# Kernel optimization log

Hardware: AMD Instinct MI355X
Metric: run time of the kernel (lower is better)

The kernel has to match this reference:

```python
import jax
import jax.numpy as jnp
from jax import lax
import numpy as np

B, N, NPOINT, NSAMPLE, C = 8, 8192, 2048, 32, 64
RADIUS = 0.2
BIG = jnp.float32(1e10)


def setup_inputs() -> dict:
    key = jax.random.key(0)
    ks = jax.random.split(key, 8)
    xyz = jax.random.uniform(ks[0], (B, N, 3), dtype=jnp.float32)          # points in unit cube
    features = jax.random.normal(ks[1], (B, C, N), dtype=jnp.float32)
    w1 = jax.random.normal(ks[2], (64, C + 3), dtype=jnp.float32) * 0.1
    b1 = jnp.zeros((64,), jnp.float32)
    w2 = jax.random.normal(ks[3], (64, 64), dtype=jnp.float32) * 0.1
    b2 = jnp.zeros((64,), jnp.float32)
    w3 = jax.random.normal(ks[4], (128, 64), dtype=jnp.float32) * 0.1
    b3 = jnp.zeros((128,), jnp.float32)
    return {"xyz": xyz, "features": features, "w1": w1, "b1": b1,
            "w2": w2, "b2": b2, "w3": w3, "b3": b3}


def _fps(xyz, npoint):
    """Furthest point sampling. xyz: (B,N,3) -> idx (B,npoint) int32."""
    def one(pts):  # (N,3)
        n = pts.shape[0]
        def step(carry, _):
            dist, far = carry
            d = jnp.sum((pts - pts[far]) ** 2, axis=-1)    # (N,)
            dist = jnp.minimum(dist, d)
            nxt = jnp.argmax(dist).astype(jnp.int32)
            return (dist, nxt), far
        init = (jnp.full((n,), BIG, pts.dtype), jnp.int32(0))
        _, idx = lax.scan(step, init, None, length=npoint)
        return idx
    return jax.vmap(one)(xyz)


def _ball_query(xyz, new_xyz, radius, nsample):
    """xyz (B,N,3), new_xyz (B,S,3) -> idx (B,S,nsample) int32, pointnet2 semantics:
    first nsample in-radius points in index order; pad with first hit."""
    n = xyz.shape[1]
    d2 = (jnp.sum(new_xyz ** 2, -1)[:, :, None]
          + jnp.sum(xyz ** 2, -1)[:, None, :]
          - 2.0 * jnp.einsum("bsd,bnd->bsn", new_xyz, xyz))  # (B,S,N)
    mask = d2 < radius * radius
    keys = jnp.where(mask, jnp.arange(n, dtype=jnp.int32)[None, None, :], jnp.int32(n))
    idx = jnp.sort(keys, axis=-1)[..., :nsample]             # (B,S,nsample)
    first = idx[..., :1]
    idx = jnp.where(idx >= n, first, idx)
    idx = jnp.where(idx >= n, 0, idx)                        # degenerate: no neighbor at all
    return idx


def _conv_bn_relu(h, w, b):
    # 1x1 Conv2d over (B, Cin, S, ns) with folded BN -> ReLU
    return jax.nn.relu(jnp.einsum("oc,bcps->bops", w, h) + b[None, :, None, None])


def _forward(xyz, features, w1, b1, w2, b2, w3, b3):
    fps_idx = _fps(xyz, NPOINT)                                          # (B,S)
    new_xyz = jnp.take_along_axis(xyz, fps_idx[:, :, None], axis=1)      # (B,S,3)
    idx = _ball_query(xyz, new_xyz, RADIUS, NSAMPLE)                     # (B,S,ns)
    b, s, ns = idx.shape
    flat = idx.reshape(b, s * ns)
    grouped_xyz = jnp.take_along_axis(xyz, flat[:, :, None], axis=1).reshape(b, s, ns, 3)
    grouped_xyz = grouped_xyz - new_xyz[:, :, None, :]                   # center
    grouped_xyz = jnp.transpose(grouped_xyz, (0, 3, 1, 2))               # (B,3,S,ns)
    grouped_feat = jnp.take_along_axis(features, flat[:, None, :], axis=2).reshape(b, C, s, ns)
    h = jnp.concatenate([grouped_xyz, grouped_feat], axis=1)             # (B,3+C,S,ns)
    h = _conv_bn_relu(h, w1, b1)
    h = _conv_bn_relu(h, w2, b2)
    h = _conv_bn_relu(h, w3, b3)
    new_features = jnp.max(h, axis=-1)                                   # (B,128,S)
    return new_xyz, new_features


def reference(xyz, features, w1, b1, w2, b2, w3, b3):
    return _forward(xyz, features, w1, b1, w2, b2, w3, b3)
```

## Files before the change

### kernel.cpp

```cpp
#include <hip/hip_runtime.h>
#include <stdint.h>

#define NB 8
#define NN 8192
#define NP 2048
#define NSAMP 32
#define NC 64

typedef float v2f __attribute__((ext_vector_type(2)));

__global__ __launch_bounds__(256) void prep_kernel(
    const float* __restrict__ w1, const float* __restrict__ w2,
    const float* __restrict__ w3, float* __restrict__ w1t,
    float* __restrict__ w2t, float* __restrict__ w3t)
{
    int j = blockIdx.x * 256 + threadIdx.x;
    if (j < 64*67) { int o = j / 67, k = j % 67; w1t[k*64 + o] = w1[j]; }
    int j2 = j - 64*67;
    if (j2 >= 0 && j2 < 64*64) { int o = j2 >> 6, k = j2 & 63; w2t[k*64 + o] = w2[j2]; }
    int j3 = j2 - 64*64;
    if (j3 >= 0 && j3 < 128*64) { int o = j3 >> 6, k = j3 & 63; w3t[k*128 + o] = w3[j3]; }
}

#define DPP_MAXF(m, CTRL) do { \
    int _s = __builtin_amdgcn_update_dpp(__float_as_int(m), __float_as_int(m), \
                                         CTRL, 0xf, 0xf, false); \
    float _f = __int_as_float(_s); \
    m = fmaxf(m, _f); } while (0)

#define DPP_MINI(c, CTRL) do { \
    int _s = __builtin_amdgcn_update_dpp(c, c, CTRL, 0xf, 0xf, false); \
    c = (_s < c) ? _s : c; } while (0)

__global__ __launch_bounds__(512) void fps_kernel(
    const float* __restrict__ xyz, int* __restrict__ fps_idx,
    float* __restrict__ out_newxyz)
{
#pragma clang fp contract(off)
    __shared__ float sxyz[NN * 3];
    __shared__ float bv[2][8];
    __shared__ int   bix[2][8];

    const int b = blockIdx.x;
    const int t = threadIdx.x;
    const int lane = t & 63;
    const int w = t >> 6;
    const float* base = xyz + (size_t)b * NN * 3;

    for (int i = t; i < NN * 3 / 4; i += 512)
        ((float4*)sxyz)[i] = ((const float4*)base)[i];
    __syncthreads();

    const int p0 = t * 16;
    v2f X[8], Y[8], Z[8], D[8];
    #pragma unroll
    for (int j = 0; j < 8; j++) {
        int pa = p0 + 2*j, pb = p0 + 2*j + 1;
        X[j] = (v2f){ sxyz[pa*3+0], sxyz[pb*3+0] };
        Y[j] = (v2f){ sxyz[pa*3+1], sxyz[pb*3+1] };
        Z[j] = (v2f){ sxyz[pa*3+2], sxyz[pb*3+2] };
        D[j] = (v2f){ 1e10f, 1e10f };
    }

    int far = 0;
    for (int k = 0; k < NP; k++) {
        float fx = sxyz[far * 3 + 0];
        float fy = sxyz[far * 3 + 1];
        float fz = sxyz[far * 3 + 2];
        if (t == 0) {
            fps_idx[b * NP + k] = far;
            out_newxyz[((size_t)b * NP + k) * 3 + 0] = fx;
            out_newxyz[((size_t)b * NP + k) * 3 + 1] = fy;
            out_newxyz[((size_t)b * NP + k) * 3 + 2] = fz;
        }

        v2f fx2 = { fx, fx }, fy2 = { fy, fy }, fz2 = { fz, fz };
        #pragma unroll
        for (int j = 0; j < 8; j++) {
            v2f dx = X[j] - fx2;
            v2f dy = Y[j] - fy2;
            v2f dz = Z[j] - fz2;
            v2f d  = (dx*dx + dy*dy) + dz*dz;
            D[j].x = fminf(D[j].x, d.x);
            D[j].y = fminf(D[j].y, d.y);
        }

        float m0 = fmaxf(fmaxf(D[0].x, D[0].y), D[1].x);
        float m1 = fmaxf(fmaxf(D[1].y, D[2].x), D[2].y);
        float m2 = fmaxf(fmaxf(D[3].x, D[3].y), D[4].x);
        float m3 = fmaxf(fmaxf(D[4].y, D[5].x), D[5].y);
        float m4 = fmaxf(fmaxf(D[6].x, D[6].y), D[7].x);
        float m  = fmaxf(fmaxf(fmaxf(m0, m1), fmaxf(m2, m3)),
                         fmaxf(m4, D[7].y));

        DPP_MAXF(m, 0x111); DPP_MAXF(m, 0x112); DPP_MAXF(m, 0x114);
        DPP_MAXF(m, 0x118); DPP_MAXF(m, 0x142); DPP_MAXF(m, 0x143);
        float wm = __int_as_float(__builtin_amdgcn_readlane(__float_as_int(m), 63));

        int cand = 0x7FFFFFFF;
        #pragma unroll
        for (int j = 7; j >= 0; j--) {
            if (D[j].y == wm) cand = p0 + 2*j + 1;
            if (D[j].x == wm) cand = p0 + 2*j;
        }
        DPP_MINI(cand, 0x111); DPP_MINI(cand, 0x112); DPP_MINI(cand, 0x114);
        DPP_MINI(cand, 0x118); DPP_MINI(cand, 0x142); DPP_MINI(cand, 0x143);
        int widx = __builtin_amdgcn_readlane(cand, 63);

        if (lane == 0) { bv[k & 1][w] = wm; bix[k & 1][w] = widx; }
        __syncthreads();

        float gv = bv[k & 1][0]; int gi = bix[k & 1][0];
        #pragma unroll
        for (int ww = 1; ww < 8; ww++) {
            float v = bv[k & 1][ww]; int i = bix[k & 1][ww];
            if (v > gv) { gv = v; gi = i; }
        }
        far = gi;
    }
}

__global__ __launch_bounds__(64) void fused_kernel(
    const float* __restrict__ xyz, const float* __restrict__ features,
    const int* __restrict__ fps_idx,
    const float* __restrict__ w1t, const float* __restrict__ b1,
    const float* __restrict__ w2t, const float* __restrict__ b2,
    const float* __restrict__ w3t, const float* __restrict__ b3,
    float* __restrict__ out_feat)
{
#pragma clang fp contract(off)
    constexpr int XP = 36;
    __shared__ __align__(16) float Xs[67 * XP];
    __shared__ __align__(16) float Hs[64 * XP];
    __shared__ int ids[NSAMP];

    const int q = blockIdx.x;
    const int b = q >> 11, s = q & (NP - 1);
    const int lane = threadIdx.x;
    const float* base = xyz + (size_t)b * NN * 3;

    int qi = fps_idx[q];
    float qx = base[qi*3+0], qy = base[qi*3+1], qz = base[qi*3+2];
    float qq = (qx*qx + qy*qy) + qz*qz;
    const float RR = 0.04f;

    int have = 0, first = 0;
    for (int c = 0; c < NN / 64; c++) {
        int p = c * 64 + lane;
        float px = base[p*3+0], py = base[p*3+1], pz = base[p*3+2];
        float pp  = (px*px + py*py) + pz*pz;
        float dot = fmaf(qz, pz, fmaf(qy, py, qx*px));
        float d2  = (qq + pp) - 2.0f*dot;
        bool pred = d2 < RR;
        unsigned long long m = __ballot(pred);
        if (have == 0 && m) first = c * 64 + (int)__builtin_ctzll(m);
        if (pred) {
            int rank = have + (int)__popcll(m & ((1ULL << lane) - 1ULL));
            if (rank < NSAMP) ids[rank] = p;
        }
        have += (int)__popcll(m);
        if (have >= NSAMP) break;
    }
    if (lane < NSAMP && lane >= have) ids[lane] = first;
    __syncthreads();

    if (lane < NSAMP) {
        int id = ids[lane];
        Xs[0*XP + lane] = base[id*3+0] - qx;
        Xs[1*XP + lane] = base[id*3+1] - qy;
        Xs[2*XP + lane] = base[id*3+2] - qz;
    }
    {
        const float* frow = features + ((size_t)b * NC + lane) * NN;
        #pragma unroll
        for (int n0 = 0; n0 < NSAMP; n0 += 4) {
            float4 v;
            v.x = frow[ids[n0+0]];
            v.y = frow[ids[n0+1]];
            v.z = frow[ids[n0+2]];
            v.w = frow[ids[n0+3]];
            *(float4*)&Xs[(3 + lane) * XP + n0] = v;
        }
    }
    __syncthreads();

    float acc[32];
    {
        float bias = b1[lane];
        #pragma unroll
        for (int n = 0; n < 32; n++) acc[n] = bias;
        for (int k = 0; k < 67; k++) {
            float w = w1t[k*64 + lane];
            const float4* xr = (const float4*)&Xs[k * XP];
            #pragma unroll
            for (int n4 = 0; n4 < 8; n4++) {
                float4 xv = xr[n4];
                acc[n4*4+0] = fmaf(w, xv.x, acc[n4*4+0]);
                acc[n4*4+1] = fmaf(w, xv.y, acc[n4*4+1]);
                acc[n4*4+2] = fmaf(w, xv.z, acc[n4*4+2]);
                acc[n4*4+3] = fmaf(w, xv.w, acc[n4*4+3]);
            }
        }
        #pragma unroll
        for (int n0 = 0; n0 < 32; n0 += 4) {
            float4 v;
            v.x = fmaxf(acc[n0+0], 0.f); v.y = fmaxf(acc[n0+1], 0.f);
            v.z = fmaxf(acc[n0+2], 0.f); v.w = fmaxf(acc[n0+3], 0.f);
            *(float4*)&Hs[lane * XP + n0] = v;
        }
    }
    __syncthreads();
    {
        float bias = b2[lane];
        #pragma unroll
        for (int n = 0; n < 32; n++) acc[n] = bias;
        for (int k = 0; k < 64; k++) {
            float w = w2t[k*64 + lane];
            const float4* xr = (const float4*)&Hs[k * XP];
            #pragma unroll
            for (int n4 = 0; n4 < 8; n4++) {
                float4 xv = xr[n4];
                acc[n4*4+0] = fmaf(w, xv.x, acc[n4*4+0]);
                acc[n4*4+1] = fmaf(w, xv.y, acc[n4*4+1]);
                acc[n4*4+2] = fmaf(w, xv.z, acc[n4*4+2]);
                acc[n4*4+3] = fmaf(w, xv.w, acc[n4*4+3]);
            }
        }
        __syncthreads();
        #pragma unroll
        for (int n0 = 0; n0 < 32; n0 += 4) {
            float4 v;
            v.x = fmaxf(acc[n0+0], 0.f); v.y = fmaxf(acc[n0+1], 0.f);
            v.z = fmaxf(acc[n0+2], 0.f); v.w = fmaxf(acc[n0+3], 0.f);
            *(float4*)&Xs[lane * XP + n0] = v;
        }
    }
    __syncthreads();
    {
        float accA[32], accB[32];
        float ba = b3[lane], bb = b3[lane + 64];
        #pragma unroll
        for (int n = 0; n < 32; n++) { accA[n] = ba; accB[n] = bb; }
        for (int k = 0; k < 64; k++) {
            float wa = w3t[k*128 + lane];
            float wb = w3t[k*128 + lane + 64];
            const float4* xr = (const float4*)&Xs[k * XP];
            #pragma unroll
            for (int n4 = 0; n4 < 8; n4++) {
                float4 xv = xr[n4];
                accA[n4*4+0] = fmaf(wa, xv.x, accA[n4*4+0]);
                accA[n4*4+1] = fmaf(wa, xv.y, accA[n4*4+1]);
                accA[n4*4+2] = fmaf(wa, xv.z, accA[n4*4+2]);
                accA[n4*4+3] = fmaf(wa, xv.w, accA[n4*4+3]);
                accB[n4*4+0] = fmaf(wb, xv.x, accB[n4*4+0]);
                accB[n4*4+1] = fmaf(wb, xv.y, accB[n4*4+1]);
                accB[n4*4+2] = fmaf(wb, xv.z, accB[n4*4+2]);
                accB[n4*4+3] = fmaf(wb, xv.w, accB[n4*4+3]);
            }
        }
        float mA = accA[0], mB = accB[0];
        #pragma unroll
        for (int n = 1; n < 32; n++) { mA = fmaxf(mA, accA[n]); mB = fmaxf(mB, accB[n]); }
        mA = fmaxf(mA, 0.f); mB = fmaxf(mB, 0.f);
        out_feat[((size_t)b*128 + lane)      * NP + s] = mA;
        out_feat[((size_t)b*128 + lane + 64) * NP + s] = mB;
    }
}

extern "C" void kernel_launch(void* const* d_in, const int* in_sizes, int n_in,
                              void* d_out, int out_size, void* d_ws, size_t ws_size,
                              hipStream_t stream)
{
    const float* xyz      = (const float*)d_in[0];
    const float* features = (const float*)d_in[1];
    const float* w1 = (const float*)d_in[2];
    const float* b1 = (const float*)d_in[3];
    const float* w2 = (const float*)d_in[4];
    const float* b2 = (const float*)d_in[5];
    const float* w3 = (const float*)d_in[6];
    const float* b3 = (const float*)d_in[7];

    float* out        = (float*)d_out;
    float* out_newxyz = out;
    float* out_feat   = out + NB * NP * 3;

    char* ws = (char*)d_ws;
    int*   fps_idx = (int*)(ws + 0);
    float* w1t     = (float*)(ws + 65536);
    float* w2t     = (float*)(ws + 82688);
    float* w3t     = (float*)(ws + 99072);

    prep_kernel<<<65, 256, 0, stream>>>(w1, w2, w3, w1t, w2t, w3t);
    fps_kernel<<<NB, 512, 0, stream>>>(xyz, fps_idx, out_newxyz);
    fused_kernel<<<NB * NP, 64, 0, stream>>>(xyz, features, fps_idx,
                                             w1t, b1, w2t, b2, w3t, b3, out_feat);
}
```

Baseline: 2.538 ms.

## Halve FPS block to 256 threads and track argmax during the distance update

The furthest-point-sampling kernel now runs 256 threads per batch, each owning 32 points instead of 16, so the cross-wave reduction covers 4 waves instead of 8. The per-thread argmax is tracked with four independent running-max chains inside the distance-update loop, which replaces the separate max tree and the equality scan for the candidate index. This is meant to cut per-iteration barrier and reduction latency in the serial 2048-step loop. In exchange each thread does twice the arithmetic per step and holds more registers, and tie-breaking relies on strict comparisons in increasing index order.

```diff
diff --git a/kernel.cpp b/kernel.cpp
--- a/kernel.cpp
+++ b/kernel.cpp
@@ -32,14 +32,14 @@
     int _s = __builtin_amdgcn_update_dpp(c, c, CTRL, 0xf, 0xf, false); \
     c = (_s < c) ? _s : c; } while (0)
 
-__global__ __launch_bounds__(512) void fps_kernel(
+__global__ __launch_bounds__(256, 1) void fps_kernel(
     const float* __restrict__ xyz, int* __restrict__ fps_idx,
     float* __restrict__ out_newxyz)
 {
 #pragma clang fp contract(off)
     __shared__ float sxyz[NN * 3];
-    __shared__ float bv[2][8];
-    __shared__ int   bix[2][8];
+    __shared__ float bv[2][4];
+    __shared__ int   bix[2][4];
 
     const int b = blockIdx.x;
     const int t = threadIdx.x;
@@ -47,14 +47,14 @@
     const int w = t >> 6;
     const float* base = xyz + (size_t)b * NN * 3;
 
-    for (int i = t; i < NN * 3 / 4; i += 512)
+    for (int i = t; i < NN * 3 / 4; i += 256)
         ((float4*)sxyz)[i] = ((const float4*)base)[i];
     __syncthreads();
 
-    const int p0 = t * 16;
-    v2f X[8], Y[8], Z[8], D[8];
+    const int p0 = t * 32;
+    v2f X[16], Y[16], Z[16], D[16];
     #pragma unroll
-    for (int j = 0; j < 8; j++) {
+    for (int j = 0; j < 16; j++) {
         int pa = p0 + 2*j, pb = p0 + 2*j + 1;
         X[j] = (v2f){ sxyz[pa*3+0], sxyz[pb*3+0] };
         Y[j] = (v2f){ sxyz[pa*3+1], sxyz[pb*3+1] };
@@ -75,34 +75,56 @@
         }
 
         v2f fx2 = { fx, fx }, fy2 = { fy, fy }, fz2 = { fz, fz };
-        #pragma unroll
-        for (int j = 0; j < 8; j++) {
-            v2f dx = X[j] - fx2;
-            v2f dy = Y[j] - fy2;
-            v2f dz = Z[j] - fz2;
+
+        float bv0 = -1.f, bv1 = -1.f, bv2 = -1.f, bv3 = -1.f;
+        int   bi0 = 0,    bi1 = 0,    bi2 = 0,    bi3 = 0;
+        #pragma unroll
+        for (int p = 0; p < 4; p++) {
+            v2f dx = X[p] - fx2, dy = Y[p] - fy2, dz = Z[p] - fz2;
             v2f d  = (dx*dx + dy*dy) + dz*dz;
-            D[j].x = fminf(D[j].x, d.x);
-            D[j].y = fminf(D[j].y, d.y);
-        }
-
-        float m0 = fmaxf(fmaxf(D[0].x, D[0].y), D[1].x);
-        float m1 = fmaxf(fmaxf(D[1].y, D[2].x), D[2].y);
-        float m2 = fmaxf(fmaxf(D[3].x, D[3].y), D[4].x);
-        float m3 = fmaxf(fmaxf(D[4].y, D[5].x), D[5].y);
-        float m4 = fmaxf(fmaxf(D[6].x, D[6].y), D[7].x);
-        float m  = fmaxf(fmaxf(fmaxf(m0, m1), fmaxf(m2, m3)),
-                         fmaxf(m4, D[7].y));
-
+            v2f nd = __builtin_elementwise_min(D[p], d);
+            D[p] = nd;
+            if (nd.x > bv0) { bv0 = nd.x; bi0 = p0 + 2*p; }
+            if (nd.y > bv0) { bv0 = nd.y; bi0 = p0 + 2*p + 1; }
+        }
+        #pragma unroll
+        for (int p = 4; p < 8; p++) {
+            v2f dx = X[p] - fx2, dy = Y[p] - fy2, dz = Z[p] - fz2;
+            v2f d  = (dx*dx + dy*dy) + dz*dz;
+            v2f nd = __builtin_elementwise_min(D[p], d);
+            D[p] = nd;
+            if (nd.x > bv1) { bv1 = nd.x; bi1 = p0 + 2*p; }
+            if (nd.y > bv1) { bv1 = nd.y; bi1 = p0 + 2*p + 1; }
+        }
+        #pragma unroll
+        for (int p = 8; p < 12; p++) {
+            v2f dx = X[p] - fx2, dy = Y[p] - fy2, dz = Z[p] - fz2;
+            v2f d  = (dx*dx + dy*dy) + dz*dz;
+            v2f nd = __builtin_elementwise_min(D[p], d);
+            D[p] = nd;
+            if (nd.x > bv2) { bv2 = nd.x; bi2 = p0 + 2*p; }
+            if (nd.y > bv2) { bv2 = nd.y; bi2 = p0 + 2*p + 1; }
+        }
+        #pragma unroll
+        for (int p = 12; p < 16; p++) {
+            v2f dx = X[p] - fx2, dy = Y[p] - fy2, dz = Z[p] - fz2;
+            v2f d  = (dx*dx + dy*dy) + dz*dz;
+            v2f nd = __builtin_elementwise_min(D[p], d);
+            D[p] = nd;
+            if (nd.x > bv3) { bv3 = nd.x; bi3 = p0 + 2*p; }
+            if (nd.y > bv3) { bv3 = nd.y; bi3 = p0 + 2*p + 1; }
+        }
+        float best = bv0; int bj = bi0;
+        if (bv1 > best) { best = bv1; bj = bi1; }
+        if (bv2 > best) { best = bv2; bj = bi2; }
+        if (bv3 > best) { best = bv3; bj = bi3; }
+
+        float m = best;
         DPP_MAXF(m, 0x111); DPP_MAXF(m, 0x112); DPP_MAXF(m, 0x114);
         DPP_MAXF(m, 0x118); DPP_MAXF(m, 0x142); DPP_MAXF(m, 0x143);
         float wm = __int_as_float(__builtin_amdgcn_readlane(__float_as_int(m), 63));
 
-        int cand = 0x7FFFFFFF;
-        #pragma unroll
-        for (int j = 7; j >= 0; j--) {
-            if (D[j].y == wm) cand = p0 + 2*j + 1;
-            if (D[j].x == wm) cand = p0 + 2*j;
-        }
+        int cand = (best == wm) ? bj : 0x7FFFFFFF;
         DPP_MINI(cand, 0x111); DPP_MINI(cand, 0x112); DPP_MINI(cand, 0x114);
         DPP_MINI(cand, 0x118); DPP_MINI(cand, 0x142); DPP_MINI(cand, 0x143);
         int widx = __builtin_amdgcn_readlane(cand, 63);
@@ -110,12 +132,14 @@
         if (lane == 0) { bv[k & 1][w] = wm; bix[k & 1][w] = widx; }
         __syncthreads();
 
-        float gv = bv[k & 1][0]; int gi = bix[k & 1][0];
-        #pragma unroll
-        for (int ww = 1; ww < 8; ww++) {
-            float v = bv[k & 1][ww]; int i = bix[k & 1][ww];
-            if (v > gv) { gv = v; gi = i; }
-        }
+        float v0 = bv[k & 1][0], v1 = bv[k & 1][1];
+        float v2 = bv[k & 1][2], v3 = bv[k & 1][3];
+        int   i0 = bix[k & 1][0], i1 = bix[k & 1][1];
+        int   i2 = bix[k & 1][2], i3 = bix[k & 1][3];
+        float gv = v0; int gi = i0;
+        if (v1 > gv) { gv = v1; gi = i1; }
+        if (v2 > gv) { gv = v2; gi = i2; }
+        if (v3 > gv) { gv = v3; gi = i3; }
         far = gi;
     }
 }
@@ -291,7 +315,7 @@
     float* w3t     = (float*)(ws + 99072);
 
     prep_kernel<<<65, 256, 0, stream>>>(w1, w2, w3, w1t, w2t, w3t);
-    fps_kernel<<<NB, 512, 0, stream>>>(xyz, fps_idx, out_newxyz);
+    fps_kernel<<<NB, 256, 0, stream>>>(xyz, fps_idx, out_newxyz);
     fused_kernel<<<NB * NP, 64, 0, stream>>>(xyz, features, fps_idx,
                                              w1t, b1, w2t, b2, w3t, b3, out_feat);
 }
```

Result: faster. 2.239 ms (-11.8%).

## Double FPS block width and track per-thread argmax during distance update

Applied to the files above, without the earlier changes.

The furthest-point-sampling kernel now runs 1024 threads per batch instead of 512, so each thread holds 8 points instead of 16. The running max and its index are tracked inline while the min-distances are updated, which replaces the separate max tree and the equality rescan. The cross-wave reduction reads 16 slots with vector loads. The goal is a shorter serial per-iteration critical path in the 2048-step loop. The cost is more waves taking part in each block barrier and a longer final reduction.

```diff
diff --git a/kernel.cpp b/kernel.cpp
--- a/kernel.cpp
+++ b/kernel.cpp
@@ -32,14 +32,14 @@
     int _s = __builtin_amdgcn_update_dpp(c, c, CTRL, 0xf, 0xf, false); \
     c = (_s < c) ? _s : c; } while (0)
 
-__global__ __launch_bounds__(512) void fps_kernel(
+__global__ __launch_bounds__(1024) void fps_kernel(
     const float* __restrict__ xyz, int* __restrict__ fps_idx,
     float* __restrict__ out_newxyz)
 {
 #pragma clang fp contract(off)
     __shared__ float sxyz[NN * 3];
-    __shared__ float bv[2][8];
-    __shared__ int   bix[2][8];
+    __shared__ __align__(16) float bv[2][16];
+    __shared__ __align__(16) int   bix[2][16];
 
     const int b = blockIdx.x;
     const int t = threadIdx.x;
@@ -47,14 +47,14 @@
     const int w = t >> 6;
     const float* base = xyz + (size_t)b * NN * 3;
 
-    for (int i = t; i < NN * 3 / 4; i += 512)
+    for (int i = t; i < NN * 3 / 4; i += 1024)
         ((float4*)sxyz)[i] = ((const float4*)base)[i];
     __syncthreads();
 
-    const int p0 = t * 16;
-    v2f X[8], Y[8], Z[8], D[8];
+    const int p0 = t * 8;
+    v2f X[4], Y[4], Z[4], D[4];
     #pragma unroll
-    for (int j = 0; j < 8; j++) {
+    for (int j = 0; j < 4; j++) {
         int pa = p0 + 2*j, pb = p0 + 2*j + 1;
         X[j] = (v2f){ sxyz[pa*3+0], sxyz[pb*3+0] };
         Y[j] = (v2f){ sxyz[pa*3+1], sxyz[pb*3+1] };
@@ -75,34 +75,36 @@
         }
 
         v2f fx2 = { fx, fx }, fy2 = { fy, fy }, fz2 = { fz, fz };
-        #pragma unroll
-        for (int j = 0; j < 8; j++) {
-            v2f dx = X[j] - fx2;
-            v2f dy = Y[j] - fy2;
-            v2f dz = Z[j] - fz2;
+
+        float bvA = -1.f, bvB = -1.f;
+        int   biA = 0,    biB = 0;
+        #pragma unroll
+        for (int p = 0; p < 2; p++) {
+            v2f dx = X[p] - fx2, dy = Y[p] - fy2, dz = Z[p] - fz2;
             v2f d  = (dx*dx + dy*dy) + dz*dz;
-            D[j].x = fminf(D[j].x, d.x);
-            D[j].y = fminf(D[j].y, d.y);
-        }
-
-        float m0 = fmaxf(fmaxf(D[0].x, D[0].y), D[1].x);
-        float m1 = fmaxf(fmaxf(D[1].y, D[2].x), D[2].y);
-        float m2 = fmaxf(fmaxf(D[3].x, D[3].y), D[4].x);
-        float m3 = fmaxf(fmaxf(D[4].y, D[5].x), D[5].y);
-        float m4 = fmaxf(fmaxf(D[6].x, D[6].y), D[7].x);
-        float m  = fmaxf(fmaxf(fmaxf(m0, m1), fmaxf(m2, m3)),
-                         fmaxf(m4, D[7].y));
-
+            v2f nd = __builtin_elementwise_min(D[p], d);
+            D[p] = nd;
+            if (nd.x > bvA) { bvA = nd.x; biA = p0 + 2*p; }
+            if (nd.y > bvA) { bvA = nd.y; biA = p0 + 2*p + 1; }
+        }
+        #pragma unroll
+        for (int p = 2; p < 4; p++) {
+            v2f dx = X[p] - fx2, dy = Y[p] - fy2, dz = Z[p] - fz2;
+            v2f d  = (dx*dx + dy*dy) + dz*dz;
+            v2f nd = __builtin_elementwise_min(D[p], d);
+            D[p] = nd;
+            if (nd.x > bvB) { bvB = nd.x; biB = p0 + 2*p; }
+            if (nd.y > bvB) { bvB = nd.y; biB = p0 + 2*p + 1; }
+        }
+        float best = bvA; int bj = biA;
+        if (bvB > best) { best = bvB; bj = biB; }
+
+        float m = best;
         DPP_MAXF(m, 0x111); DPP_MAXF(m, 0x112); DPP_MAXF(m, 0x114);
         DPP_MAXF(m, 0x118); DPP_MAXF(m, 0x142); DPP_MAXF(m, 0x143);
         float wm = __int_as_float(__builtin_amdgcn_readlane(__float_as_int(m), 63));
 
-        int cand = 0x7FFFFFFF;
-        #pragma unroll
-        for (int j = 7; j >= 0; j--) {
-            if (D[j].y == wm) cand = p0 + 2*j + 1;
-            if (D[j].x == wm) cand = p0 + 2*j;
-        }
+        int cand = (best == wm) ? bj : 0x7FFFFFFF;
         DPP_MINI(cand, 0x111); DPP_MINI(cand, 0x112); DPP_MINI(cand, 0x114);
         DPP_MINI(cand, 0x118); DPP_MINI(cand, 0x142); DPP_MINI(cand, 0x143);
         int widx = __builtin_amdgcn_readlane(cand, 63);
@@ -110,11 +112,17 @@
         if (lane == 0) { bv[k & 1][w] = wm; bix[k & 1][w] = widx; }
         __syncthreads();
 
-        float gv = bv[k & 1][0]; int gi = bix[k & 1][0];
-        #pragma unroll
-        for (int ww = 1; ww < 8; ww++) {
-            float v = bv[k & 1][ww]; int i = bix[k & 1][ww];
-            if (v > gv) { gv = v; gi = i; }
+        const float4* pv = (const float4*)bv[k & 1];
+        const int4*   pi = (const int4*)bix[k & 1];
+        float gv = -1.f; int gi = 0;
+        #pragma unroll
+        for (int g = 0; g < 4; g++) {
+            float4 vv = pv[g];
+            int4   ii = pi[g];
+            if (vv.x > gv) { gv = vv.x; gi = ii.x; }
+            if (vv.y > gv) { gv = vv.y; gi = ii.y; }
+            if (vv.z > gv) { gv = vv.z; gi = ii.z; }
+            if (vv.w > gv) { gv = vv.w; gi = ii.w; }
         }
         far = gi;
     }
@@ -291,7 +299,7 @@
     float* w3t     = (float*)(ws + 99072);
 
     prep_kernel<<<65, 256, 0, stream>>>(w1, w2, w3, w1t, w2t, w3t);
-    fps_kernel<<<NB, 512, 0, stream>>>(xyz, fps_idx, out_newxyz);
+    fps_kernel<<<NB, 1024, 0, stream>>>(xyz, fps_idx, out_newxyz);
     fused_kernel<<<NB * NP, 64, 0, stream>>>(xyz, features, fps_idx,
                                              w1t, b1, w2t, b2, w3t, b3, out_feat);
 }
```

Result: slower. 3.092 ms (+21.8%).
